# Optimization experiments

Measured on AMD Instinct MI355X. Metric: run time of the kernel, lower is better.

The kernel has to match this reference:

```python
import jax, jax.numpy as jnp
import numpy as np

B, S, D, H = 2, 2048, 1024, 16
HD = D // H  # 64

def setup_inputs() -> dict:
    key = jax.random.key(0)
    ks = jax.random.split(key, 6)
    s = 1.0 / np.sqrt(D)
    return {
        "x": jax.random.normal(ks[0], (B, S, D), dtype=jnp.float32),
        "wq": jax.random.normal(ks[1], (D, D), dtype=jnp.float32) * s,
        "wk": jax.random.normal(ks[2], (D, D), dtype=jnp.float32) * s,
        "wv": jax.random.normal(ks[3], (D, D), dtype=jnp.float32) * s,
        "wo": jax.random.normal(ks[4], (D, D), dtype=jnp.float32) * s,
        "bo": jax.random.normal(ks[5], (D,), dtype=jnp.float32) * 0.01,
    }

def reference(x, wq, wk, wv, wo, bo):
    b, s, _ = x.shape
    # QKV projections (qkvBias=False), reshape to [b, h, s, hd]
    q = (x @ wq).reshape(b, s, H, HD).transpose(0, 2, 1, 3)
    k = (x @ wk).reshape(b, s, H, HD).transpose(0, 2, 1, 3)
    v = (x @ wv).reshape(b, s, H, HD).transpose(0, 2, 1, 3)
    # scores, causal mask (upper triangle -> -inf), scale, softmax
    scores = jnp.einsum('bhqd,bhkd->bhqk', q, k)
    causal = jnp.triu(jnp.ones((s, s), dtype=bool), k=1)
    scores = jnp.where(causal, -jnp.inf, scores) / np.sqrt(HD)
    weights = jax.nn.softmax(scores, axis=-1)  # dropout=0 (eval)
    ctx = jnp.einsum('bhqk,bhkd->bhqd', weights, v)
    ctx = ctx.transpose(0, 2, 1, 3).reshape(b, s, D)
    return ctx @ wo + bo
```

## Files before the change

kernel.cpp:

```cpp
#include <hip/hip_runtime.h>
#include <hip/hip_bf16.h>
#include <math.h>

#define BB 2
#define SS 2048
#define DD 1024
#define HH 16
#define HDIM 64

typedef unsigned short u16;
typedef __attribute__((ext_vector_type(8))) short bfrag;
typedef __attribute__((ext_vector_type(4))) float f32x4;

#define NEG_BIG (-1e30f)
#define QSCALE 0.18033688011112042f

__device__ __forceinline__ u16 f2u(float f) {
    unsigned int u = __builtin_bit_cast(unsigned int, f);
    u += 0x7fffu + ((u >> 16) & 1u);
    return (u16)(u >> 16);
}

__device__ __forceinline__ void async16(const u16* g, u16* l) {
    __builtin_amdgcn_global_load_lds((__attribute__((address_space(1))) void*)g,
                                     (__attribute__((address_space(3))) void*)l,
                                     16, 0, 0);
}

__device__ __forceinline__ f32x4 mfma16(bfrag a, bfrag b, f32x4 c) {
    return __builtin_amdgcn_mfma_f32_16x16x32_bf16(a, b, c, 0, 0, 0);
}

__global__ __launch_bounds__(256) void prep_k(
    const float* __restrict__ x,  u16* __restrict__ xb,
    const float* __restrict__ wq, const float* __restrict__ wk,
    const float* __restrict__ wv, const float* __restrict__ wo,
    u16* __restrict__ wT)
{
    const int id = blockIdx.x;
    const int t = threadIdx.x;
    if (id < 2048) {
        int i = (id * 256 + t) * 8;
        float4 a = *(const float4*)(x + i);
        float4 b = *(const float4*)(x + i + 4);
        u16 o[8] = { f2u(a.x), f2u(a.y), f2u(a.z), f2u(a.w),
                     f2u(b.x), f2u(b.y), f2u(b.z), f2u(b.w) };
        *(uint4*)(xb + i) = *(uint4*)o;
        return;
    }
    const int wid = id - 2048;
    const int z = wid >> 8;
    const int kt = wid & 15, nt = (wid >> 4) & 15;
    const float* w = (z == 0) ? wq : (z == 1) ? wk : (z == 2) ? wv : wo;
    u16* o = wT + (size_t)z * DD * DD;
    __shared__ __align__(16) u16 T[64][72];
    const int k0 = kt * 64, n0 = nt * 64;
    {
        int kr = t >> 2, nb = (t & 3) * 16;
        const float4* s4 = (const float4*)(w + (size_t)(k0 + kr) * DD + n0 + nb);
        #pragma unroll
        for (int jj = 0; jj < 4; ++jj) {
            float4 v = s4[jj];
            T[kr][nb + jj*4 + 0] = f2u(v.x);
            T[kr][nb + jj*4 + 1] = f2u(v.y);
            T[kr][nb + jj*4 + 2] = f2u(v.z);
            T[kr][nb + jj*4 + 3] = f2u(v.w);
        }
    }
    __syncthreads();
    {
        int nr = t >> 2, kb = (t & 3) * 16;
        u16 tmp[16];
        #pragma unroll
        for (int j = 0; j < 16; ++j) tmp[j] = T[kb + j][nr];
        *(uint4*)(o + (size_t)(n0 + nr) * DD + k0 + kb)     = ((uint4*)tmp)[0];
        *(uint4*)(o + (size_t)(n0 + nr) * DD + k0 + kb + 8) = ((uint4*)tmp)[1];
    }
}

__global__ __launch_bounds__(256) void gemm_qkv_k(
    const u16* __restrict__ xb, const u16* __restrict__ wT,
    u16* __restrict__ Qo, u16* __restrict__ Ko, u16* __restrict__ Vt)
{
    const u16* wTz = wT + (size_t)blockIdx.z * DD * DD;
    const float osc = (blockIdx.z == 0) ? QSCALE : 1.0f;

    __shared__ __align__(16) u16 As[128 * 64];
    __shared__ __align__(16) u16 Bs[128 * 64];

    const int t = threadIdx.x;
    const int m0 = blockIdx.x * 128, n0 = blockIdx.y * 128;
    const int lane15 = t & 15, quad = (t >> 4) & 3, wave = t >> 6;
    const int wm = wave & 1, wn = wave >> 1;

    int srow[4], scol[4];
    #pragma unroll
    for (int i = 0; i < 4; ++i) {
        int c = t + i * 256;
        srow[i] = c >> 3;
        scol[i] = (c & 7) ^ (srow[i] & 7);
    }
    const int ldb = (t & 192) * 8;

    int aoff[4][2], boff[4][2];
    #pragma unroll
    for (int mi = 0; mi < 4; ++mi) {
        int r = wm * 64 + mi * 16 + lane15;
        #pragma unroll
        for (int kh = 0; kh < 2; ++kh)
            aoff[mi][kh] = (r * 8 + ((kh * 4 + quad) ^ (r & 7))) * 8;
    }
    #pragma unroll
    for (int ni = 0; ni < 4; ++ni) {
        int r = wn * 64 + ni * 16 + lane15;
        #pragma unroll
        for (int kh = 0; kh < 2; ++kh)
            boff[ni][kh] = (r * 8 + ((kh * 4 + quad) ^ (r & 7))) * 8;
    }

    f32x4 acc[4][4];
    #pragma unroll
    for (int mi = 0; mi < 4; ++mi)
        #pragma unroll
        for (int ni = 0; ni < 4; ++ni)
            acc[mi][ni] = (f32x4){0.f, 0.f, 0.f, 0.f};

    for (int it = 0; it < 16; ++it) {
        const int k0 = it * 64;
        #pragma unroll
        for (int i = 0; i < 4; ++i) {
            async16(xb  + (size_t)(m0 + srow[i]) * DD + k0 + scol[i] * 8,
                    As + ldb + i * 2048);
            async16(wTz + (size_t)(n0 + srow[i]) * DD + k0 + scol[i] * 8,
                    Bs + ldb + i * 2048);
        }
        __syncthreads();
        #pragma unroll
        for (int kh = 0; kh < 2; ++kh) {
            bfrag av[4], bv[4];
            #pragma unroll
            for (int mi = 0; mi < 4; ++mi) av[mi] = *(const bfrag*)(As + aoff[mi][kh]);
            #pragma unroll
            for (int ni = 0; ni < 4; ++ni) bv[ni] = *(const bfrag*)(Bs + boff[ni][kh]);
            #pragma unroll
            for (int mi = 0; mi < 4; ++mi)
                #pragma unroll
                for (int ni = 0; ni < 4; ++ni)
                    acc[mi][ni] = mfma16(av[mi], bv[ni], acc[mi][ni]);
        }
        __syncthreads();
    }

    if (blockIdx.z != 2) {
        u16* out = (blockIdx.z == 0) ? Qo : Ko;
        #pragma unroll
        for (int mi = 0; mi < 4; ++mi) {
            #pragma unroll
            for (int r = 0; r < 4; ++r) {
                int m = m0 + wm * 64 + mi * 16 + quad * 4 + r;
                int b = m >> 11, s = m & (SS - 1);
                #pragma unroll
                for (int ni = 0; ni < 4; ++ni) {
                    int n = n0 + wn * 64 + ni * 16 + lane15;
                    int h = n >> 6, hd = n & 63;
                    out[(((size_t)(b * HH + h)) * SS + s) * HDIM + hd] = f2u(acc[mi][ni][r] * osc);
                }
            }
        }
    } else {
        u16* T = As;
        const int bq = m0 >> 11;
        const int ms = m0 & (SS - 1);
        #pragma unroll
        for (int hh = 0; hh < 2; ++hh) {
            if (wn == hh) {
                #pragma unroll
                for (int mi = 0; mi < 4; ++mi)
                    #pragma unroll
                    for (int r = 0; r < 4; ++r) {
                        int ml = wm * 64 + mi * 16 + quad * 4 + r;
                        #pragma unroll
                        for (int ni = 0; ni < 4; ++ni) {
                            int nl = ni * 16 + lane15;
                            T[nl * 128 + (ml ^ ((nl & 7) << 4))] = f2u(acc[mi][ni][r]);
                        }
                    }
            }
            __syncthreads();
            const int h = (n0 >> 6) + hh;
            u16* dst = Vt + ((size_t)(bq * HH + h)) * (HDIM * SS);
            #pragma unroll
            for (int i = 0; i < 4; ++i) {
                int c = t + i * 256;
                int row = c >> 4;
                int mb  = (c & 15) * 8;
                uint4 val = *(const uint4*)&T[row * 128 + (mb ^ ((row & 7) << 4))];
                *(uint4*)(dst + (size_t)row * SS + ms + mb) = val;
            }
            __syncthreads();
        }
    }
}

__global__ __launch_bounds__(256) void gemm_out_k(
    const u16* __restrict__ ctxb, const u16* __restrict__ woT,
    const float* __restrict__ bo, float* __restrict__ out)
{
    __shared__ __align__(16) u16 As[128 * 64];
    __shared__ __align__(16) u16 Bs[64 * 64];

    const int t = threadIdx.x;
    const int m0 = blockIdx.x * 128, n0 = blockIdx.y * 64;
    const int lane15 = t & 15, quad = (t >> 4) & 3, wave = t >> 6;
    const int wm = wave & 1, wn = wave >> 1;

    int srow[4], scol[4];
    #pragma unroll
    for (int i = 0; i < 4; ++i) {
        int c = t + i * 256;
        srow[i] = c >> 3;
        scol[i] = (c & 7) ^ (srow[i] & 7);
    }
    const int ldb = (t & 192) * 8;

    int aoff[4][2], boff[2][2];
    #pragma unroll
    for (int mi = 0; mi < 4; ++mi) {
        int r = wm * 64 + mi * 16 + lane15;
        #pragma unroll
        for (int kh = 0; kh < 2; ++kh)
            aoff[mi][kh] = (r * 8 + ((kh * 4 + quad) ^ (r & 7))) * 8;
    }
    #pragma unroll
    for (int ni = 0; ni < 2; ++ni) {
        int r = wn * 32 + ni * 16 + lane15;
        #pragma unroll
        for (int kh = 0; kh < 2; ++kh)
            boff[ni][kh] = (r * 8 + ((kh * 4 + quad) ^ (r & 7))) * 8;
    }

    f32x4 acc[4][2];
    #pragma unroll
    for (int mi = 0; mi < 4; ++mi)
        #pragma unroll
        for (int ni = 0; ni < 2; ++ni)
            acc[mi][ni] = (f32x4){0.f, 0.f, 0.f, 0.f};

    for (int it = 0; it < 16; ++it) {
        const int k0 = it * 64;
        #pragma unroll
        for (int i = 0; i < 4; ++i)
            async16(ctxb + (size_t)(m0 + srow[i]) * DD + k0 + scol[i] * 8,
                    As + ldb + i * 2048);
        #pragma unroll
        for (int i = 0; i < 2; ++i)
            async16(woT + (size_t)(n0 + srow[i]) * DD + k0 + scol[i] * 8,
                    Bs + ldb + i * 2048);
        __syncthreads();
        #pragma unroll
        for (int kh = 0; kh < 2; ++kh) {
            bfrag av[4], bv[2];
            #pragma unroll
            for (int mi = 0; mi < 4; ++mi) av[mi] = *(const bfrag*)(As + aoff[mi][kh]);
            #pragma unroll
            for (int ni = 0; ni < 2; ++ni) bv[ni] = *(const bfrag*)(Bs + boff[ni][kh]);
            #pragma unroll
            for (int mi = 0; mi < 4; ++mi)
                #pragma unroll
                for (int ni = 0; ni < 2; ++ni)
                    acc[mi][ni] = mfma16(av[mi], bv[ni], acc[mi][ni]);
        }
        __syncthreads();
    }

    float bias[2];
    #pragma unroll
    for (int ni = 0; ni < 2; ++ni)
        bias[ni] = bo[n0 + wn * 32 + ni * 16 + lane15];

    #pragma unroll
    for (int mi = 0; mi < 4; ++mi) {
        #pragma unroll
        for (int r = 0; r < 4; ++r) {
            int m = m0 + wm * 64 + mi * 16 + quad * 4 + r;
            #pragma unroll
            for (int ni = 0; ni < 2; ++ni) {
                int n = n0 + wn * 32 + ni * 16 + lane15;
                out[(size_t)m * DD + n] = acc[mi][ni][r] + bias[ni];
            }
        }
    }
}

__global__ __launch_bounds__(256, 4) void attn_k(
    const u16* __restrict__ Q, const u16* __restrict__ K,
    const u16* __restrict__ Vt, u16* __restrict__ ctx)
{
    __shared__ __align__(16) u16 QP[64 * 64];
    __shared__ __align__(16) u16 Ks[2][64 * 64];
    __shared__ __align__(16) u16 Vs[2][64 * 64];

    const int t = threadIdx.x;
    const int lane15 = t & 15, quad = (t >> 4) & 3, wave = t >> 6;
    const int bh = blockIdx.x;
    const int qt = (int)(gridDim.y - 1) - (int)blockIdx.y;
    const int q0 = qt * 64;
    const int b = bh >> 4, h = bh & 15;

    const u16* Qb = Q  + (size_t)bh * SS * HDIM;
    const u16* Kb = K  + (size_t)bh * SS * HDIM;
    const u16* Vb = Vt + (size_t)bh * HDIM * SS;

    const int kr0 = t >> 3,         ks0 = t & 7;
    const int kr1 = (t + 256) >> 3, ks1 = (t + 256) & 7;
    const int kc0 = ks0 ^ (kr0 & 7);
    const int kc1 = ks1 ^ (kr1 & 7);
    const int ldst = (t & 192) * 8;

    async16(Qb + (size_t)(q0 + kr0) * HDIM + kc0 * 8, QP + ldst);
    async16(Qb + (size_t)(q0 + kr1) * HDIM + kc1 * 8, QP + ldst + 2048);
    async16(Kb + (size_t)kr0 * HDIM + kc0 * 8, &Ks[0][ldst]);
    async16(Kb + (size_t)kr1 * HDIM + kc1 * 8, &Ks[0][ldst + 2048]);
    async16(Vb + (size_t)kr0 * SS + kc0 * 8, &Vs[0][ldst]);
    async16(Vb + (size_t)kr1 * SS + kc1 * 8, &Vs[0][ldst + 2048]);

    const int qrow = wave * 16 + lane15;
    int qoff[2], koff[4][2];
    #pragma unroll
    for (int kh = 0; kh < 2; ++kh)
        qoff[kh] = (qrow * 8 + ((kh * 4 + quad) ^ (qrow & 7))) * 8;
    #pragma unroll
    for (int ni = 0; ni < 4; ++ni)
        #pragma unroll
        for (int kh = 0; kh < 2; ++kh) {
            int row = ni * 16 + lane15;
            koff[ni][kh] = (row * 8 + ((kh * 4 + quad) ^ (row & 7))) * 8;
        }

    __syncthreads();
    bfrag aq[2];
    aq[0] = *(const bfrag*)(QP + qoff[0]);
    aq[1] = *(const bfrag*)(QP + qoff[1]);
    __syncthreads();

    f32x4 acc_o[4];
    float rsum[4] = {0.f, 0.f, 0.f, 0.f};
    #pragma unroll
    for (int nd = 0; nd < 4; ++nd) acc_o[nd] = (f32x4){0.f, 0.f, 0.f, 0.f};

    const int qgb = q0 + wave * 16 + quad * 4;

    for (int kt = 0; kt <= qt; ++kt) {
        if (kt < qt) {
            const int nv0 = (kt + 1) * 64;
            const int pb = (kt + 1) & 1;
            async16(Kb + (size_t)(nv0 + kr0) * HDIM + kc0 * 8, &Ks[pb][ldst]);
            async16(Kb + (size_t)(nv0 + kr1) * HDIM + kc1 * 8, &Ks[pb][ldst + 2048]);
            async16(Vb + (size_t)kr0 * SS + nv0 + kc0 * 8, &Vs[pb][ldst]);
            async16(Vb + (size_t)kr1 * SS + nv0 + kc1 * 8, &Vs[pb][ldst + 2048]);
        }
        const int cb = kt & 1;
        const int kv0 = kt * 64;

        f32x4 s_acc[4];
        #pragma unroll
        for (int ni = 0; ni < 4; ++ni) s_acc[ni] = (f32x4){0.f, 0.f, 0.f, 0.f};
        #pragma unroll
        for (int kh = 0; kh < 2; ++kh)
            #pragma unroll
            for (int ni = 0; ni < 4; ++ni)
                s_acc[ni] = mfma16(aq[kh], *(const bfrag*)&Ks[cb][koff[ni][kh]], s_acc[ni]);

        const bool diag = (kt == qt);
        #pragma unroll
        for (int ni = 0; ni < 4; ++ni) {
            int kvg = kv0 + ni * 16 + lane15;
            #pragma unroll
            for (int r = 0; r < 4; ++r) {
                float v = s_acc[ni][r];
                if (diag && (kvg > qgb + r)) v = NEG_BIG;
                float pw = exp2f(v);
                unsigned pu = __builtin_bit_cast(unsigned, pw);
                rsum[r] += __builtin_bit_cast(float, pu & 0xffff0000u);
                int row = wave * 16 + quad * 4 + r;
                int col = ni * 16 + lane15;
                QP[(row * 8 + ((col >> 3) ^ (row & 7))) * 8 + (col & 7)] = (u16)(pu >> 16);
            }
        }

        #pragma unroll
        for (int kh = 0; kh < 2; ++kh) {
            bfrag ap = *(const bfrag*)(QP + qoff[kh]);
            #pragma unroll
            for (int nd = 0; nd < 4; ++nd)
                acc_o[nd] = mfma16(ap, *(const bfrag*)&Vs[cb][koff[nd][kh]], acc_o[nd]);
        }
        __syncthreads();
    }

    #pragma unroll
    for (int off = 1; off < 16; off <<= 1)
        #pragma unroll
        for (int r = 0; r < 4; ++r)
            rsum[r] += __shfl_xor(rsum[r], off, 64);

    #pragma unroll
    for (int r = 0; r < 4; ++r) {
        float inv = 1.f / rsum[r];
        int srow = q0 + wave * 16 + quad * 4 + r;
        size_t base = ((size_t)b * SS + srow) * DD + h * HDIM;
        #pragma unroll
        for (int nd = 0; nd < 4; ++nd)
            ctx[base + nd * 16 + lane15] = f2u(acc_o[nd][r] * inv);
    }
}

extern "C" void kernel_launch(void* const* d_in, const int* in_sizes, int n_in,
                              void* d_out, int out_size, void* d_ws, size_t ws_size,
                              hipStream_t stream) {
    const float* x  = (const float*)d_in[0];
    const float* wq = (const float*)d_in[1];
    const float* wk = (const float*)d_in[2];
    const float* wv = (const float*)d_in[3];
    const float* wo = (const float*)d_in[4];
    const float* bo = (const float*)d_in[5];
    float* out = (float*)d_out;

    char* ws = (char*)d_ws;
    const size_t MB8 = (size_t)8 * 1024 * 1024;
    u16* xb  = (u16*)(ws);
    u16* wT  = (u16*)(ws + MB8);
    u16* Qb  = (u16*)(ws + 2 * MB8);
    u16* Kb  = (u16*)(ws + 3 * MB8);
    u16* Vt  = (u16*)(ws + 4 * MB8);
    u16* ctxb = xb;

    prep_k  <<<3072, 256, 0, stream>>>(x, xb, wq, wk, wv, wo, wT);
    gemm_qkv_k<<<dim3(32, 8, 3), 256, 0, stream>>>(xb, wT, Qb, Kb, Vt);
    attn_k  <<<dim3(32, 32), 256, 0, stream>>>(Qb, Kb, Vt, ctxb);
    gemm_out_k<<<dim3(32, 16), 256, 0, stream>>>(ctxb, wT + (size_t)3 * DD * DD, bo, out);
}
```

Before: 182.5 us.

## Fuse all four stages into one persistent cooperative kernel with grid syncs

```diff
diff --git a/kernel.cpp b/kernel.cpp
--- a/kernel.cpp
+++ b/kernel.cpp
@@ -1,6 +1,9 @@
 #include <hip/hip_runtime.h>
+#include <hip/hip_cooperative_groups.h>
 #include <hip/hip_bf16.h>
 #include <math.h>
+
+namespace cg = cooperative_groups;
 
 #define BB 2
 #define SS 2048
@@ -29,6 +32,388 @@
 
 __device__ __forceinline__ f32x4 mfma16(bfrag a, bfrag b, f32x4 c) {
     return __builtin_amdgcn_mfma_f32_16x16x32_bf16(a, b, c, 0, 0, 0);
+}
+
+__global__ __launch_bounds__(256, 4) void fused_k(
+    const float* __restrict__ x,
+    const float* __restrict__ wq, const float* __restrict__ wk,
+    const float* __restrict__ wv, const float* __restrict__ wo,
+    const float* __restrict__ bo,
+    u16* __restrict__ xb, u16* __restrict__ wT,
+    u16* __restrict__ Qb, u16* __restrict__ Kb, u16* __restrict__ Vt,
+    float* __restrict__ out)
+{
+    cg::grid_group grid = cg::this_grid();
+    __shared__ __align__(16) u16 smem[20480];
+    const int t = threadIdx.x;
+    const int gsz = (int)gridDim.x;
+    const int lane15 = t & 15, quad = (t >> 4) & 3, wave = t >> 6;
+
+    for (int id = blockIdx.x; id < 3072; id += gsz) {
+        if (id < 2048) {
+            int i = (id * 256 + t) * 8;
+            float4 a = *(const float4*)(x + i);
+            float4 b = *(const float4*)(x + i + 4);
+            u16 o8[8] = { f2u(a.x), f2u(a.y), f2u(a.z), f2u(a.w),
+                          f2u(b.x), f2u(b.y), f2u(b.z), f2u(b.w) };
+            *(uint4*)(xb + i) = *(uint4*)o8;
+        } else {
+            const int wid = id - 2048;
+            const int z = wid >> 8;
+            const int ktt = wid & 15, ntt = (wid >> 4) & 15;
+            const float* w = (z == 0) ? wq : (z == 1) ? wk : (z == 2) ? wv : wo;
+            u16* o = wT + (size_t)z * DD * DD;
+            u16 (*T)[72] = (u16(*)[72])smem;
+            const int k0 = ktt * 64, n0 = ntt * 64;
+            {
+                int kr = t >> 2, nbs = (t & 3) * 16;
+                const float4* s4 = (const float4*)(w + (size_t)(k0 + kr) * DD + n0 + nbs);
+                #pragma unroll
+                for (int jj = 0; jj < 4; ++jj) {
+                    float4 v = s4[jj];
+                    T[kr][nbs + jj*4 + 0] = f2u(v.x);
+                    T[kr][nbs + jj*4 + 1] = f2u(v.y);
+                    T[kr][nbs + jj*4 + 2] = f2u(v.z);
+                    T[kr][nbs + jj*4 + 3] = f2u(v.w);
+                }
+            }
+            __syncthreads();
+            {
+                int nr = t >> 2, kb2 = (t & 3) * 16;
+                u16 tmp[16];
+                #pragma unroll
+                for (int j = 0; j < 16; ++j) tmp[j] = T[kb2 + j][nr];
+                *(uint4*)(o + (size_t)(n0 + nr) * DD + k0 + kb2)     = ((uint4*)tmp)[0];
+                *(uint4*)(o + (size_t)(n0 + nr) * DD + k0 + kb2 + 8) = ((uint4*)tmp)[1];
+            }
+        }
+        __syncthreads();
+    }
+    grid.sync();
+
+    for (int id = blockIdx.x; id < 768; id += gsz) {
+        const int z = id >> 8;
+        const int m0 = (id & 31) * 128, n0 = ((id >> 5) & 7) * 128;
+        const u16* wTz = wT + (size_t)z * DD * DD;
+        const float osc = (z == 0) ? QSCALE : 1.0f;
+        u16* As = smem;
+        u16* Bs = smem + 8192;
+        const int wm = wave & 1, wn = wave >> 1;
+
+        int srow[4], scol[4];
+        #pragma unroll
+        for (int i = 0; i < 4; ++i) {
+            int c = t + i * 256;
+            srow[i] = c >> 3;
+            scol[i] = (c & 7) ^ (srow[i] & 7);
+        }
+        const int ldb = (t & 192) * 8;
+
+        int aoff[4][2], boff[4][2];
+        #pragma unroll
+        for (int mi = 0; mi < 4; ++mi) {
+            int r = wm * 64 + mi * 16 + lane15;
+            #pragma unroll
+            for (int kh = 0; kh < 2; ++kh)
+                aoff[mi][kh] = (r * 8 + ((kh * 4 + quad) ^ (r & 7))) * 8;
+        }
+        #pragma unroll
+        for (int ni = 0; ni < 4; ++ni) {
+            int r = wn * 64 + ni * 16 + lane15;
+            #pragma unroll
+            for (int kh = 0; kh < 2; ++kh)
+                boff[ni][kh] = (r * 8 + ((kh * 4 + quad) ^ (r & 7))) * 8;
+        }
+
+        f32x4 acc[4][4];
+        #pragma unroll
+        for (int mi = 0; mi < 4; ++mi)
+            #pragma unroll
+            for (int ni = 0; ni < 4; ++ni)
+                acc[mi][ni] = (f32x4){0.f, 0.f, 0.f, 0.f};
+
+        for (int it = 0; it < 16; ++it) {
+            const int k0 = it * 64;
+            #pragma unroll
+            for (int i = 0; i < 4; ++i) {
+                async16(xb  + (size_t)(m0 + srow[i]) * DD + k0 + scol[i] * 8,
+                        As + ldb + i * 2048);
+                async16(wTz + (size_t)(n0 + srow[i]) * DD + k0 + scol[i] * 8,
+                        Bs + ldb + i * 2048);
+            }
+            __syncthreads();
+            #pragma unroll
+            for (int kh = 0; kh < 2; ++kh) {
+                bfrag av[4], bv[4];
+                #pragma unroll
+                for (int mi = 0; mi < 4; ++mi) av[mi] = *(const bfrag*)(As + aoff[mi][kh]);
+                #pragma unroll
+                for (int ni = 0; ni < 4; ++ni) bv[ni] = *(const bfrag*)(Bs + boff[ni][kh]);
+                #pragma unroll
+                for (int mi = 0; mi < 4; ++mi)
+                    #pragma unroll
+                    for (int ni = 0; ni < 4; ++ni)
+                        acc[mi][ni] = mfma16(av[mi], bv[ni], acc[mi][ni]);
+            }
+            __syncthreads();
+        }
+
+        if (z != 2) {
+            u16* o = (z == 0) ? Qb : Kb;
+            #pragma unroll
+            for (int mi = 0; mi < 4; ++mi) {
+                #pragma unroll
+                for (int r = 0; r < 4; ++r) {
+                    int m = m0 + wm * 64 + mi * 16 + quad * 4 + r;
+                    int b = m >> 11, s = m & (SS - 1);
+                    #pragma unroll
+                    for (int ni = 0; ni < 4; ++ni) {
+                        int n = n0 + wn * 64 + ni * 16 + lane15;
+                        int h = n >> 6, hd = n & 63;
+                        o[(((size_t)(b * HH + h)) * SS + s) * HDIM + hd] = f2u(acc[mi][ni][r] * osc);
+                    }
+                }
+            }
+            __syncthreads();
+        } else {
+            u16* T = smem;
+            const int bq = m0 >> 11;
+            const int ms = m0 & (SS - 1);
+            #pragma unroll
+            for (int hh = 0; hh < 2; ++hh) {
+                if (wn == hh) {
+                    #pragma unroll
+                    for (int mi = 0; mi < 4; ++mi)
+                        #pragma unroll
+                        for (int r = 0; r < 4; ++r) {
+                            int ml = wm * 64 + mi * 16 + quad * 4 + r;
+                            #pragma unroll
+                            for (int ni = 0; ni < 4; ++ni) {
+                                int nl = ni * 16 + lane15;
+                                T[nl * 128 + (ml ^ ((nl & 7) << 4))] = f2u(acc[mi][ni][r]);
+                            }
+                        }
+                }
+                __syncthreads();
+                const int h = (n0 >> 6) + hh;
+                u16* dst = Vt + ((size_t)(bq * HH + h)) * (HDIM * SS);
+                #pragma unroll
+                for (int i = 0; i < 4; ++i) {
+                    int c = t + i * 256;
+                    int row = c >> 4;
+                    int mb  = (c & 15) * 8;
+                    uint4 val = *(const uint4*)&T[row * 128 + (mb ^ ((row & 7) << 4))];
+                    *(uint4*)(dst + (size_t)row * SS + ms + mb) = val;
+                }
+                __syncthreads();
+            }
+        }
+    }
+    grid.sync();
+
+    for (int id = blockIdx.x; id < 1024; id += gsz) {
+        const int kk = id >> 8, j = id & 255;
+        const int bh = j >> 3, p = j & 7;
+        const int qt = kk * 8 + ((kk & 1) ? (7 - p) : p);
+        const int q0 = qt * 64;
+        const int b = bh >> 4, h = bh & 15;
+
+        const u16* Qp = Qb + (size_t)bh * SS * HDIM;
+        const u16* Kp = Kb + (size_t)bh * SS * HDIM;
+        const u16* Vp = Vt + (size_t)bh * HDIM * SS;
+        u16* QP = smem;
+
+        const int kr0 = t >> 3,         ks0 = t & 7;
+        const int kr1 = (t + 256) >> 3, ks1 = (t + 256) & 7;
+        const int kc0 = ks0 ^ (kr0 & 7);
+        const int kc1 = ks1 ^ (kr1 & 7);
+        const int ldst = (t & 192) * 8;
+
+        async16(Qp + (size_t)(q0 + kr0) * HDIM + kc0 * 8, QP + ldst);
+        async16(Qp + (size_t)(q0 + kr1) * HDIM + kc1 * 8, QP + ldst + 2048);
+        async16(Kp + (size_t)kr0 * HDIM + kc0 * 8, smem + 4096 + ldst);
+        async16(Kp + (size_t)kr1 * HDIM + kc1 * 8, smem + 4096 + ldst + 2048);
+        async16(Vp + (size_t)kr0 * SS + kc0 * 8, smem + 12288 + ldst);
+        async16(Vp + (size_t)kr1 * SS + kc1 * 8, smem + 12288 + ldst + 2048);
+
+        const int qrow = wave * 16 + lane15;
+        int qoff[2], koff[4][2];
+        #pragma unroll
+        for (int kh = 0; kh < 2; ++kh)
+            qoff[kh] = (qrow * 8 + ((kh * 4 + quad) ^ (qrow & 7))) * 8;
+        #pragma unroll
+        for (int ni = 0; ni < 4; ++ni)
+            #pragma unroll
+            for (int kh = 0; kh < 2; ++kh) {
+                int row = ni * 16 + lane15;
+                koff[ni][kh] = (row * 8 + ((kh * 4 + quad) ^ (row & 7))) * 8;
+            }
+
+        __syncthreads();
+        bfrag aq[2];
+        aq[0] = *(const bfrag*)(QP + qoff[0]);
+        aq[1] = *(const bfrag*)(QP + qoff[1]);
+        __syncthreads();
+
+        f32x4 acc_o[4];
+        float rsum[4] = {0.f, 0.f, 0.f, 0.f};
+        #pragma unroll
+        for (int nd = 0; nd < 4; ++nd) acc_o[nd] = (f32x4){0.f, 0.f, 0.f, 0.f};
+
+        const int qgb = q0 + wave * 16 + quad * 4;
+
+        for (int kt = 0; kt <= qt; ++kt) {
+            if (kt < qt) {
+                const int nv0 = (kt + 1) * 64;
+                const int pb = (kt + 1) & 1;
+                async16(Kp + (size_t)(nv0 + kr0) * HDIM + kc0 * 8, smem + 4096 + pb * 4096 + ldst);
+                async16(Kp + (size_t)(nv0 + kr1) * HDIM + kc1 * 8, smem + 4096 + pb * 4096 + ldst + 2048);
+                async16(Vp + (size_t)kr0 * SS + nv0 + kc0 * 8, smem + 12288 + pb * 4096 + ldst);
+                async16(Vp + (size_t)kr1 * SS + nv0 + kc1 * 8, smem + 12288 + pb * 4096 + ldst + 2048);
+            }
+            const u16* ksb = smem + 4096 + (kt & 1) * 4096;
+            const u16* vsb = smem + 12288 + (kt & 1) * 4096;
+            const int kv0 = kt * 64;
+
+            f32x4 s_acc[4];
+            #pragma unroll
+            for (int ni = 0; ni < 4; ++ni) s_acc[ni] = (f32x4){0.f, 0.f, 0.f, 0.f};
+            #pragma unroll
+            for (int kh = 0; kh < 2; ++kh)
+                #pragma unroll
+                for (int ni = 0; ni < 4; ++ni)
+                    s_acc[ni] = mfma16(aq[kh], *(const bfrag*)(ksb + koff[ni][kh]), s_acc[ni]);
+
+            const bool diag = (kt == qt);
+            #pragma unroll
+            for (int ni = 0; ni < 4; ++ni) {
+                int kvg = kv0 + ni * 16 + lane15;
+                #pragma unroll
+                for (int r = 0; r < 4; ++r) {
+                    float v = s_acc[ni][r];
+                    if (diag && (kvg > qgb + r)) v = NEG_BIG;
+                    float pw = exp2f(v);
+                    unsigned pu = __builtin_bit_cast(unsigned, pw);
+                    rsum[r] += __builtin_bit_cast(float, pu & 0xffff0000u);
+                    int row = wave * 16 + quad * 4 + r;
+                    int col = ni * 16 + lane15;
+                    QP[(row * 8 + ((col >> 3) ^ (row & 7))) * 8 + (col & 7)] = (u16)(pu >> 16);
+                }
+            }
+
+            #pragma unroll
+            for (int kh = 0; kh < 2; ++kh) {
+                bfrag ap = *(const bfrag*)(QP + qoff[kh]);
+                #pragma unroll
+                for (int nd = 0; nd < 4; ++nd)
+                    acc_o[nd] = mfma16(ap, *(const bfrag*)(vsb + koff[nd][kh]), acc_o[nd]);
+            }
+            __syncthreads();
+        }
+
+        #pragma unroll
+        for (int off = 1; off < 16; off <<= 1)
+            #pragma unroll
+            for (int r = 0; r < 4; ++r)
+                rsum[r] += __shfl_xor(rsum[r], off, 64);
+
+        #pragma unroll
+        for (int r = 0; r < 4; ++r) {
+            float inv = 1.f / rsum[r];
+            int srw = q0 + wave * 16 + quad * 4 + r;
+            size_t base = ((size_t)b * SS + srw) * DD + h * HDIM;
+            #pragma unroll
+            for (int nd = 0; nd < 4; ++nd)
+                xb[base + nd * 16 + lane15] = f2u(acc_o[nd][r] * inv);
+        }
+        __syncthreads();
+    }
+    grid.sync();
+
+    for (int id = blockIdx.x; id < 512; id += gsz) {
+        const int m0 = (id & 31) * 128, n0 = (id >> 5) * 64;
+        const u16* woT = wT + (size_t)3 * DD * DD;
+        u16* As = smem;
+        u16* Bs = smem + 8192;
+        const int wm = wave & 1, wn = wave >> 1;
+
+        int srow[4], scol[4];
+        #pragma unroll
+        for (int i = 0; i < 4; ++i) {
+            int c = t + i * 256;
+            srow[i] = c >> 3;
+            scol[i] = (c & 7) ^ (srow[i] & 7);
+        }
+        const int ldb = (t & 192) * 8;
+
+        int aoff[4][2], boff[2][2];
+        #pragma unroll
+        for (int mi = 0; mi < 4; ++mi) {
+            int r = wm * 64 + mi * 16 + lane15;
+            #pragma unroll
+            for (int kh = 0; kh < 2; ++kh)
+                aoff[mi][kh] = (r * 8 + ((kh * 4 + quad) ^ (r & 7))) * 8;
+        }
+        #pragma unroll
+        for (int ni = 0; ni < 2; ++ni) {
+            int r = wn * 32 + ni * 16 + lane15;
+            #pragma unroll
+            for (int kh = 0; kh < 2; ++kh)
+                boff[ni][kh] = (r * 8 + ((kh * 4 + quad) ^ (r & 7))) * 8;
+        }
+
+        f32x4 acc[4][2];
+        #pragma unroll
+        for (int mi = 0; mi < 4; ++mi)
+            #pragma unroll
+            for (int ni = 0; ni < 2; ++ni)
+                acc[mi][ni] = (f32x4){0.f, 0.f, 0.f, 0.f};
+
+        for (int it = 0; it < 16; ++it) {
+            const int k0 = it * 64;
+            #pragma unroll
+            for (int i = 0; i < 4; ++i)
+                async16(xb + (size_t)(m0 + srow[i]) * DD + k0 + scol[i] * 8,
+                        As + ldb + i * 2048);
+            #pragma unroll
+            for (int i = 0; i < 2; ++i)
+                async16(woT + (size_t)(n0 + srow[i]) * DD + k0 + scol[i] * 8,
+                        Bs + ldb + i * 2048);
+            __syncthreads();
+            #pragma unroll
+            for (int kh = 0; kh < 2; ++kh) {
+                bfrag av[4], bv[2];
+                #pragma unroll
+                for (int mi = 0; mi < 4; ++mi) av[mi] = *(const bfrag*)(As + aoff[mi][kh]);
+                #pragma unroll
+                for (int ni = 0; ni < 2; ++ni) bv[ni] = *(const bfrag*)(Bs + boff[ni][kh]);
+                #pragma unroll
+                for (int mi = 0; mi < 4; ++mi)
+                    #pragma unroll
+                    for (int ni = 0; ni < 2; ++ni)
+                        acc[mi][ni] = mfma16(av[mi], bv[ni], acc[mi][ni]);
+            }
+            __syncthreads();
+        }
+
+        float bias[2];
+        #pragma unroll
+        for (int ni = 0; ni < 2; ++ni)
+            bias[ni] = bo[n0 + wn * 32 + ni * 16 + lane15];
+
+        #pragma unroll
+        for (int mi = 0; mi < 4; ++mi) {
+            #pragma unroll
+            for (int r = 0; r < 4; ++r) {
+                int m = m0 + wm * 64 + mi * 16 + quad * 4 + r;
+                #pragma unroll
+                for (int ni = 0; ni < 2; ++ni) {
+                    int n = n0 + wn * 32 + ni * 16 + lane15;
+                    out[(size_t)m * DD + n] = acc[mi][ni][r] + bias[ni];
+                }
+            }
+        }
+    }
 }
 
 __global__ __launch_bounds__(256) void prep_k(
@@ -84,15 +469,12 @@
 {
     const u16* wTz = wT + (size_t)blockIdx.z * DD * DD;
     const float osc = (blockIdx.z == 0) ? QSCALE : 1.0f;
-
     __shared__ __align__(16) u16 As[128 * 64];
     __shared__ __align__(16) u16 Bs[128 * 64];
-
     const int t = threadIdx.x;
     const int m0 = blockIdx.x * 128, n0 = blockIdx.y * 128;
     const int lane15 = t & 15, quad = (t >> 4) & 3, wave = t >> 6;
     const int wm = wave & 1, wn = wave >> 1;
-
     int srow[4], scol[4];
     #pragma unroll
     for (int i = 0; i < 4; ++i) {
@@ -101,7 +483,6 @@
         scol[i] = (c & 7) ^ (srow[i] & 7);
     }
     const int ldb = (t & 192) * 8;
-
     int aoff[4][2], boff[4][2];
     #pragma unroll
     for (int mi = 0; mi < 4; ++mi) {
@@ -117,22 +498,18 @@
         for (int kh = 0; kh < 2; ++kh)
             boff[ni][kh] = (r * 8 + ((kh * 4 + quad) ^ (r & 7))) * 8;
     }
-
     f32x4 acc[4][4];
     #pragma unroll
     for (int mi = 0; mi < 4; ++mi)
         #pragma unroll
         for (int ni = 0; ni < 4; ++ni)
             acc[mi][ni] = (f32x4){0.f, 0.f, 0.f, 0.f};
-
     for (int it = 0; it < 16; ++it) {
         const int k0 = it * 64;
         #pragma unroll
         for (int i = 0; i < 4; ++i) {
-            async16(xb  + (size_t)(m0 + srow[i]) * DD + k0 + scol[i] * 8,
-                    As + ldb + i * 2048);
-            async16(wTz + (size_t)(n0 + srow[i]) * DD + k0 + scol[i] * 8,
-                    Bs + ldb + i * 2048);
+            async16(xb  + (size_t)(m0 + srow[i]) * DD + k0 + scol[i] * 8, As + ldb + i * 2048);
+            async16(wTz + (size_t)(n0 + srow[i]) * DD + k0 + scol[i] * 8, Bs + ldb + i * 2048);
         }
         __syncthreads();
         #pragma unroll
@@ -150,11 +527,10 @@
         }
         __syncthreads();
     }
-
     if (blockIdx.z != 2) {
         u16* out = (blockIdx.z == 0) ? Qo : Ko;
         #pragma unroll
-        for (int mi = 0; mi < 4; ++mi) {
+        for (int mi = 0; mi < 4; ++mi)
             #pragma unroll
             for (int r = 0; r < 4; ++r) {
                 int m = m0 + wm * 64 + mi * 16 + quad * 4 + r;
@@ -166,7 +542,6 @@
                     out[(((size_t)(b * HH + h)) * SS + s) * HDIM + hd] = f2u(acc[mi][ni][r] * osc);
                 }
             }
-        }
     } else {
         u16* T = As;
         const int bq = m0 >> 11;
@@ -208,12 +583,10 @@
 {
     __shared__ __align__(16) u16 As[128 * 64];
     __shared__ __align__(16) u16 Bs[64 * 64];
-
     const int t = threadIdx.x;
     const int m0 = blockIdx.x * 128, n0 = blockIdx.y * 64;
     const int lane15 = t & 15, quad = (t >> 4) & 3, wave = t >> 6;
     const int wm = wave & 1, wn = wave >> 1;
-
     int srow[4], scol[4];
     #pragma unroll
     for (int i = 0; i < 4; ++i) {
@@ -222,7 +595,6 @@
         scol[i] = (c & 7) ^ (srow[i] & 7);
     }
     const int ldb = (t & 192) * 8;
-
     int aoff[4][2], boff[2][2];
     #pragma unroll
     for (int mi = 0; mi < 4; ++mi) {
@@ -238,24 +610,20 @@
         for (int kh = 0; kh < 2; ++kh)
             boff[ni][kh] = (r * 8 + ((kh * 4 + quad) ^ (r & 7))) * 8;
     }
-
     f32x4 acc[4][2];
     #pragma unroll
     for (int mi = 0; mi < 4; ++mi)
         #pragma unroll
         for (int ni = 0; ni < 2; ++ni)
             acc[mi][ni] = (f32x4){0.f, 0.f, 0.f, 0.f};
-
     for (int it = 0; it < 16; ++it) {
         const int k0 = it * 64;
         #pragma unroll
         for (int i = 0; i < 4; ++i)
-            async16(ctxb + (size_t)(m0 + srow[i]) * DD + k0 + scol[i] * 8,
-                    As + ldb + i * 2048);
+            async16(ctxb + (size_t)(m0 + srow[i]) * DD + k0 + scol[i] * 8, As + ldb + i * 2048);
         #pragma unroll
         for (int i = 0; i < 2; ++i)
-            async16(woT + (size_t)(n0 + srow[i]) * DD + k0 + scol[i] * 8,
-                    Bs + ldb + i * 2048);
+            async16(woT + (size_t)(n0 + srow[i]) * DD + k0 + scol[i] * 8, Bs + ldb + i * 2048);
         __syncthreads();
         #pragma unroll
         for (int kh = 0; kh < 2; ++kh) {
@@ -272,14 +640,12 @@
         }
         __syncthreads();
     }
-
     float bias[2];
     #pragma unroll
     for (int ni = 0; ni < 2; ++ni)
         bias[ni] = bo[n0 + wn * 32 + ni * 16 + lane15];
-
-    #pragma unroll
-    for (int mi = 0; mi < 4; ++mi) {
+    #pragma unroll
+    for (int mi = 0; mi < 4; ++mi)
         #pragma unroll
         for (int r = 0; r < 4; ++r) {
             int m = m0 + wm * 64 + mi * 16 + quad * 4 + r;
@@ -289,7 +655,6 @@
                 out[(size_t)m * DD + n] = acc[mi][ni][r] + bias[ni];
             }
         }
-    }
 }
 
 __global__ __launch_bounds__(256, 4) void attn_k(
@@ -299,31 +664,26 @@
     __shared__ __align__(16) u16 QP[64 * 64];
     __shared__ __align__(16) u16 Ks[2][64 * 64];
     __shared__ __align__(16) u16 Vs[2][64 * 64];
-
     const int t = threadIdx.x;
     const int lane15 = t & 15, quad = (t >> 4) & 3, wave = t >> 6;
     const int bh = blockIdx.x;
     const int qt = (int)(gridDim.y - 1) - (int)blockIdx.y;
     const int q0 = qt * 64;
     const int b = bh >> 4, h = bh & 15;
-
     const u16* Qb = Q  + (size_t)bh * SS * HDIM;
     const u16* Kb = K  + (size_t)bh * SS * HDIM;
     const u16* Vb = Vt + (size_t)bh * HDIM * SS;
-
     const int kr0 = t >> 3,         ks0 = t & 7;
     const int kr1 = (t + 256) >> 3, ks1 = (t + 256) & 7;
     const int kc0 = ks0 ^ (kr0 & 7);
     const int kc1 = ks1 ^ (kr1 & 7);
     const int ldst = (t & 192) * 8;
-
     async16(Qb + (size_t)(q0 + kr0) * HDIM + kc0 * 8, QP + ldst);
     async16(Qb + (size_t)(q0 + kr1) * HDIM + kc1 * 8, QP + ldst + 2048);
     async16(Kb + (size_t)kr0 * HDIM + kc0 * 8, &Ks[0][ldst]);
     async16(Kb + (size_t)kr1 * HDIM + kc1 * 8, &Ks[0][ldst + 2048]);
     async16(Vb + (size_t)kr0 * SS + kc0 * 8, &Vs[0][ldst]);
     async16(Vb + (size_t)kr1 * SS + kc1 * 8, &Vs[0][ldst + 2048]);
-
     const int qrow = wave * 16 + lane15;
     int qoff[2], koff[4][2];
     #pragma unroll
@@ -336,20 +696,16 @@
             int row = ni * 16 + lane15;
             koff[ni][kh] = (row * 8 + ((kh * 4 + quad) ^ (row & 7))) * 8;
         }
-
     __syncthreads();
     bfrag aq[2];
     aq[0] = *(const bfrag*)(QP + qoff[0]);
     aq[1] = *(const bfrag*)(QP + qoff[1]);
     __syncthreads();
-
     f32x4 acc_o[4];
     float rsum[4] = {0.f, 0.f, 0.f, 0.f};
     #pragma unroll
     for (int nd = 0; nd < 4; ++nd) acc_o[nd] = (f32x4){0.f, 0.f, 0.f, 0.f};
-
     const int qgb = q0 + wave * 16 + quad * 4;
-
     for (int kt = 0; kt <= qt; ++kt) {
         if (kt < qt) {
             const int nv0 = (kt + 1) * 64;
@@ -361,7 +717,6 @@
         }
         const int cb = kt & 1;
         const int kv0 = kt * 64;
-
         f32x4 s_acc[4];
         #pragma unroll
         for (int ni = 0; ni < 4; ++ni) s_acc[ni] = (f32x4){0.f, 0.f, 0.f, 0.f};
@@ -370,7 +725,6 @@
             #pragma unroll
             for (int ni = 0; ni < 4; ++ni)
                 s_acc[ni] = mfma16(aq[kh], *(const bfrag*)&Ks[cb][koff[ni][kh]], s_acc[ni]);
-
         const bool diag = (kt == qt);
         #pragma unroll
         for (int ni = 0; ni < 4; ++ni) {
@@ -387,7 +741,6 @@
                 QP[(row * 8 + ((col >> 3) ^ (row & 7))) * 8 + (col & 7)] = (u16)(pu >> 16);
             }
         }
-
         #pragma unroll
         for (int kh = 0; kh < 2; ++kh) {
             bfrag ap = *(const bfrag*)(QP + qoff[kh]);
@@ -397,13 +750,11 @@
         }
         __syncthreads();
     }
-
     #pragma unroll
     for (int off = 1; off < 16; off <<= 1)
         #pragma unroll
         for (int r = 0; r < 4; ++r)
             rsum[r] += __shfl_xor(rsum[r], off, 64);
-
     #pragma unroll
     for (int r = 0; r < 4; ++r) {
         float inv = 1.f / rsum[r];
@@ -433,10 +784,23 @@
     u16* Qb  = (u16*)(ws + 2 * MB8);
     u16* Kb  = (u16*)(ws + 3 * MB8);
     u16* Vt  = (u16*)(ws + 4 * MB8);
-    u16* ctxb = xb;
-
-    prep_k  <<<3072, 256, 0, stream>>>(x, xb, wq, wk, wv, wo, wT);
-    gemm_qkv_k<<<dim3(32, 8, 3), 256, 0, stream>>>(xb, wT, Qb, Kb, Vt);
-    attn_k  <<<dim3(32, 32), 256, 0, stream>>>(Qb, Kb, Vt, ctxb);
-    gemm_out_k<<<dim3(32, 16), 256, 0, stream>>>(ctxb, wT + (size_t)3 * DD * DD, bo, out);
+
+    int occ = 0;
+    hipError_t qe = hipOccupancyMaxActiveBlocksPerMultiprocessor(&occ, (const void*)fused_k, 256, 0);
+    if (qe != hipSuccess || occ < 1) occ = 1;
+    int grid = occ * 256;
+    if (grid > 1024) grid = 1024;
+
+    void* args[] = { (void*)&x, (void*)&wq, (void*)&wk, (void*)&wv, (void*)&wo,
+                     (void*)&bo, (void*)&xb, (void*)&wT, (void*)&Qb, (void*)&Kb,
+                     (void*)&Vt, (void*)&out };
+    hipError_t e = hipLaunchCooperativeKernel((const void*)fused_k, dim3(grid), dim3(256),
+                                              args, 0, stream);
+    if (e != hipSuccess) {
+        u16* ctxb = xb;
+        prep_k   <<<3072, 256, 0, stream>>>(x, xb, wq, wk, wv, wo, wT);
+        gemm_qkv_k<<<dim3(32, 8, 3), 256, 0, stream>>>(xb, wT, Qb, Kb, Vt);
+        attn_k   <<<dim3(32, 32), 256, 0, stream>>>(Qb, Kb, Vt, ctxb);
+        gemm_out_k<<<dim3(32, 16), 256, 0, stream>>>(ctxb, wT + (size_t)3 * DD * DD, bo, out);
+    }
 }
```

New measurement: 416.2 us. +128.1%, slower.
